# Performance work log

Measured on AMD Instinct MI355X. Metric: run time of the kernel, lower is better.

## Reference

```python
import jax, jax.numpy as jnp
import numpy as np

D_MODEL = 1024
NUM_HEADS = 16
HEAD_DIM = D_MODEL // NUM_HEADS  # 64
B, S = 4, 2048


def setup_inputs() -> dict:
    key = jax.random.key(0)
    ks = jax.random.split(key, 10)
    scale = 1.0 / np.sqrt(D_MODEL)
    x = jax.random.normal(ks[0], (B, S, D_MODEL), dtype=jnp.float32)
    # per-head projection weights stacked over the head axis (matches ModuleList of Linears)
    Wq = jax.random.normal(ks[1], (NUM_HEADS, D_MODEL, HEAD_DIM), dtype=jnp.float32) * scale
    bq = jax.random.normal(ks[2], (NUM_HEADS, HEAD_DIM), dtype=jnp.float32) * 0.01
    Wk = jax.random.normal(ks[3], (NUM_HEADS, D_MODEL, HEAD_DIM), dtype=jnp.float32) * scale
    bk = jax.random.normal(ks[4], (NUM_HEADS, HEAD_DIM), dtype=jnp.float32) * 0.01
    Wv = jax.random.normal(ks[5], (NUM_HEADS, D_MODEL, HEAD_DIM), dtype=jnp.float32) * scale
    bv = jax.random.normal(ks[6], (NUM_HEADS, HEAD_DIM), dtype=jnp.float32) * 0.01
    Wo = jax.random.normal(ks[7], (D_MODEL, D_MODEL), dtype=jnp.float32) * scale
    bo = jax.random.normal(ks[8], (D_MODEL,), dtype=jnp.float32) * 0.01
    return {"hidden_state": x, "Wq": Wq, "bq": bq, "Wk": Wk, "bk": bk,
            "Wv": Wv, "bv": bv, "Wo": Wo, "bo": bo}


def reference(hidden_state, Wq, bq, Wk, bk, Wv, bv, Wo, bo):
    # q,k,v: [B, H, S, E]
    q = jnp.einsum('bsd,hde->bhse', hidden_state, Wq) + bq[None, :, None, :]
    k = jnp.einsum('bsd,hde->bhse', hidden_state, Wk) + bk[None, :, None, :]
    v = jnp.einsum('bsd,hde->bhse', hidden_state, Wv) + bv[None, :, None, :]
    scores = jnp.einsum('bhse,bhte->bhst', q, k) / jnp.sqrt(jnp.asarray(HEAD_DIM, q.dtype))
    weights = jax.nn.softmax(scores, axis=-1)  # [B, H, S, S]
    attn = jnp.einsum('bhst,bhte->bhse', weights, v)  # [B, H, S, E]
    # concat heads along feature dim (head order preserved)
    attn = jnp.transpose(attn, (0, 2, 1, 3)).reshape(hidden_state.shape[0], hidden_state.shape[1], D_MODEL)
    return attn @ Wo + bo
```

## Files before the change

### kernel.cpp

```cpp
#include <hip/hip_runtime.h>

typedef __bf16 bf16x8 __attribute__((ext_vector_type(8)));
typedef float f32x4 __attribute__((ext_vector_type(4)));
typedef unsigned int u32x4 __attribute__((ext_vector_type(4)));
typedef unsigned int u32x2 __attribute__((ext_vector_type(2)));
typedef unsigned short u16x8 __attribute__((ext_vector_type(8)));

#define MFMA_BF16(a, b, c) __builtin_amdgcn_mfma_f32_16x16x32_bf16((a), (b), (c), 0, 0, 0)

#define QSCALE 0.18033688011112043f

__device__ __forceinline__ unsigned short f2bf(float f) {
    unsigned int u = __builtin_bit_cast(unsigned int, f);
    u += 0x7FFFu + ((u >> 16) & 1u);
    return (unsigned short)(u >> 16);
}

__device__ __forceinline__ unsigned int pack_bf16_rne(float a, float b) {
    unsigned int ua = __builtin_bit_cast(unsigned int, a);
    unsigned int ub = __builtin_bit_cast(unsigned int, b);
    ua += 0x7FFFu + ((ua >> 16) & 1u);
    ub += 0x7FFFu + ((ub >> 16) & 1u);
    return __builtin_amdgcn_perm(ub, ua, 0x07060302);
}

#if __has_builtin(__builtin_amdgcn_cvt_pk_bf16_f32)
typedef __bf16 bf16x2 __attribute__((ext_vector_type(2)));
__device__ __forceinline__ unsigned int pack_bf16(float a, float b) {
    return __builtin_bit_cast(unsigned int, __builtin_amdgcn_cvt_pk_bf16_f32(a, b));
}
#else
__device__ __forceinline__ unsigned int pack_bf16(float a, float b) {
    return pack_bf16_rne(a, b);
}
#endif

#if __has_builtin(__builtin_amdgcn_exp2f)
__device__ __forceinline__ float fast_exp2(float x) { return __builtin_amdgcn_exp2f(x); }
#else
__device__ __forceinline__ float fast_exp2(float x) {
    float r;
    asm("v_exp_f32 %0, %1\n\ts_nop 0" : "=v"(r) : "v"(x));
    return r;
}
#endif

__device__ __forceinline__ bf16x8 ldfrag(const unsigned short* p) {
    return __builtin_bit_cast(bf16x8, *(const u32x4*)p);
}

typedef const __attribute__((address_space(1))) void* gas_t;
typedef __attribute__((address_space(3))) void* las_t;
__device__ __forceinline__ void dma16(const unsigned short* g, unsigned short* l) {
    __builtin_amdgcn_global_load_lds((gas_t)(const void*)g, (las_t)(void*)l, 16, 0, 0);
}

__device__ __forceinline__ void pipeline_barrier() {
    __builtin_amdgcn_s_waitcnt(0);
    __syncthreads();
}


__global__ void cvt_x_kernel(const float* __restrict__ in, unsigned short* __restrict__ out) {
    long long t = (long long)blockIdx.x * 256 + threadIdx.x;
    const f32x4* p = (const f32x4*)in + t * 2;
    f32x4 v0 = p[0], v1 = p[1];
    u16x8 o;
    o[0] = f2bf(v0[0]); o[1] = f2bf(v0[1]); o[2] = f2bf(v0[2]); o[3] = f2bf(v0[3]);
    o[4] = f2bf(v1[0]); o[5] = f2bf(v1[1]); o[6] = f2bf(v1[2]); o[7] = f2bf(v1[3]);
    *((u16x8*)out + t) = o;
}

__global__ void cvt_wqkvT_kernel(const float* __restrict__ Wq, const float* __restrict__ Wk,
                                 const float* __restrict__ Wv, unsigned short* __restrict__ WT) {
    int n = blockIdx.x * 256 + threadIdx.x;
    int d0 = blockIdx.y * 8;
    int proj = n >> 10, rem = n & 1023, h = rem >> 6, e = rem & 63;
    const float* W = (proj == 0) ? Wq : (proj == 1) ? Wk : Wv;
    const float* src = W + (size_t)h * 65536 + (size_t)d0 * 64 + e;
    u16x8 o;
#pragma unroll
    for (int j = 0; j < 8; j++) o[j] = f2bf(src[j * 64]);
    *(u16x8*)(WT + (size_t)n * 1024 + d0) = o;
}

__global__ void cvt_woT_kernel(const float* __restrict__ Wo, unsigned short* __restrict__ WoT) {
    int n = blockIdx.x * 256 + threadIdx.x;
    int d0 = blockIdx.y * 8;
    const float* src = Wo + (size_t)d0 * 1024 + n;
    u16x8 o;
#pragma unroll
    for (int j = 0; j < 8; j++) o[j] = f2bf(src[j * 1024]);
    *(u16x8*)(WoT + (size_t)n * 1024 + d0) = o;
}


__global__ __launch_bounds__(256) void gemm_qkv_kernel(
    const unsigned short* __restrict__ A, const unsigned short* __restrict__ BT,
    const float* __restrict__ bq, const float* __restrict__ bk, const float* __restrict__ bv,
    unsigned short* __restrict__ Qo, unsigned short* __restrict__ Ko, unsigned short* __restrict__ VTo) {
    __shared__ unsigned short As[2 * 128 * 32];
    __shared__ unsigned short Bs[2 * 128 * 32];
    const int tid = threadIdx.x;
    const int m0 = blockIdx.y * 128, n0 = blockIdx.x * 128;
    const int w = tid >> 6, lane = tid & 63, lr = lane & 15, quad = lane >> 4;
    const int wy = w >> 1, wx = w & 1;
    f32x4 acc[4][4];
#pragma unroll
    for (int i = 0; i < 4; i++)
#pragma unroll
        for (int j = 0; j < 4; j++) acc[i][j] = (f32x4){0.f, 0.f, 0.f, 0.f};
    const int drow = lane >> 2;
    const int dchunk = (lane & 3) ^ (drow & 3);
    const unsigned short* gA = A + (size_t)(m0 + w * 32 + drow) * 1024 + dchunk * 8;
    const unsigned short* gB = BT + (size_t)(n0 + w * 32 + drow) * 1024 + dchunk * 8;
    const int swav = (w * 32) * 32;
    const int fcol = (quad ^ (lr & 3)) * 8;
    dma16(gA, As + swav);
    dma16(gA + 16 * 1024, As + swav + 16 * 32);
    dma16(gB, Bs + swav);
    dma16(gB + 16 * 1024, Bs + swav + 16 * 32);
#pragma unroll 2
    for (int k0 = 0; k0 < 1024; k0 += 32) {
        const int cur = (k0 >> 5) & 1;
        const unsigned short* cA = As + cur * 4096;
        const unsigned short* cB = Bs + cur * 4096;
        pipeline_barrier();
        bf16x8 af[4], bfr[4];
#pragma unroll
        for (int i = 0; i < 4; i++) af[i] = ldfrag(cA + (wy * 64 + i * 16 + lr) * 32 + fcol);
#pragma unroll
        for (int j = 0; j < 4; j++) bfr[j] = ldfrag(cB + (wx * 64 + j * 16 + lr) * 32 + fcol);
        if (k0 + 32 < 1024) {
            const int nb = (cur ^ 1) * 4096 + swav;
            dma16(gA + k0 + 32, As + nb);
            dma16(gA + k0 + 32 + 16 * 1024, As + nb + 16 * 32);
            dma16(gB + k0 + 32, Bs + nb);
            dma16(gB + k0 + 32 + 16 * 1024, Bs + nb + 16 * 32);
        }
#pragma unroll
        for (int i = 0; i < 4; i++)
#pragma unroll
            for (int j = 0; j < 4; j++) acc[i][j] = MFMA_BF16(af[i], bfr[j], acc[i][j]);
    }
#pragma unroll
    for (int j = 0; j < 4; j++) {
        int n = n0 + wx * 64 + j * 16 + lr;
        int proj = n >> 10, rem = n & 1023, h = rem >> 6, e = rem & 63;
        if (proj == 2) {
            float bb = bv[rem];
#pragma unroll
            for (int i = 0; i < 4; i++) {
                int m = m0 + wy * 64 + i * 16 + quad * 4;
                int batch = m >> 11, s = m & 2047;
                u32x2 pk;
                pk[0] = pack_bf16_rne(acc[i][j][0] + bb, acc[i][j][1] + bb);
                pk[1] = pack_bf16_rne(acc[i][j][2] + bb, acc[i][j][3] + bb);
                *(u32x2*)(VTo + (((size_t)batch * 16 + h) * 64 + e) * 2048 + s) = pk;
            }
        } else {
            const float* bias = (proj == 0) ? bq : bk;
            unsigned short* dst = (proj == 0) ? Qo : Ko;
            float bb = bias[rem];
            float scl = (proj == 0) ? QSCALE : 1.0f;
#pragma unroll
            for (int i = 0; i < 4; i++) {
#pragma unroll
                for (int r = 0; r < 4; r++) {
                    int m = m0 + wy * 64 + i * 16 + quad * 4 + r;
                    int batch = m >> 11, s = m & 2047;
                    dst[(((size_t)batch * 16 + h) * 2048 + s) * 64 + e] = f2bf((acc[i][j][r] + bb) * scl);
                }
            }
        }
    }
}

__global__ __launch_bounds__(256) void gemm_out_kernel(
    const unsigned short* __restrict__ A, const unsigned short* __restrict__ BT,
    const float* __restrict__ bo, float* __restrict__ out) {
    __shared__ unsigned short As[2 * 128 * 32];
    __shared__ unsigned short Bs[2 * 128 * 32];
    const int tid = threadIdx.x;
    const int m0 = blockIdx.y * 128, n0 = blockIdx.x * 128;
    const int w = tid >> 6, lane = tid & 63, lr = lane & 15, quad = lane >> 4;
    const int wy = w >> 1, wx = w & 1;
    f32x4 acc[4][4];
#pragma unroll
    for (int i = 0; i < 4; i++)
#pragma unroll
        for (int j = 0; j < 4; j++) acc[i][j] = (f32x4){0.f, 0.f, 0.f, 0.f};
    const int drow = lane >> 2;
    const int dchunk = (lane & 3) ^ (drow & 3);
    const unsigned short* gA = A + (size_t)(m0 + w * 32 + drow) * 1024 + dchunk * 8;
    const unsigned short* gB = BT + (size_t)(n0 + w * 32 + drow) * 1024 + dchunk * 8;
    const int swav = (w * 32) * 32;
    const int fcol = (quad ^ (lr & 3)) * 8;
    dma16(gA, As + swav);
    dma16(gA + 16 * 1024, As + swav + 16 * 32);
    dma16(gB, Bs + swav);
    dma16(gB + 16 * 1024, Bs + swav + 16 * 32);
#pragma unroll 2
    for (int k0 = 0; k0 < 1024; k0 += 32) {
        const int cur = (k0 >> 5) & 1;
        const unsigned short* cA = As + cur * 4096;
        const unsigned short* cB = Bs + cur * 4096;
        pipeline_barrier();
        bf16x8 af[4], bfr[4];
#pragma unroll
        for (int i = 0; i < 4; i++) af[i] = ldfrag(cA + (wy * 64 + i * 16 + lr) * 32 + fcol);
#pragma unroll
        for (int j = 0; j < 4; j++) bfr[j] = ldfrag(cB + (wx * 64 + j * 16 + lr) * 32 + fcol);
        if (k0 + 32 < 1024) {
            const int nb = (cur ^ 1) * 4096 + swav;
            dma16(gA + k0 + 32, As + nb);
            dma16(gA + k0 + 32 + 16 * 1024, As + nb + 16 * 32);
            dma16(gB + k0 + 32, Bs + nb);
            dma16(gB + k0 + 32 + 16 * 1024, Bs + nb + 16 * 32);
        }
#pragma unroll
        for (int i = 0; i < 4; i++)
#pragma unroll
            for (int j = 0; j < 4; j++) acc[i][j] = MFMA_BF16(af[i], bfr[j], acc[i][j]);
    }
#pragma unroll
    for (int j = 0; j < 4; j++) {
        int n = n0 + wx * 64 + j * 16 + lr;
        float bb = bo[n];
#pragma unroll
        for (int i = 0; i < 4; i++) {
#pragma unroll
            for (int r = 0; r < 4; r++) {
                int m = m0 + wy * 64 + i * 16 + quad * 4 + r;
                out[(size_t)m * 1024 + n] = acc[i][j][r] + bb;
            }
        }
    }
}

#define ST 72
__global__ __launch_bounds__(256, 2) void attn_fa_kernel(
    const unsigned short* __restrict__ Q, const unsigned short* __restrict__ K,
    const unsigned short* __restrict__ VT, unsigned short* __restrict__ Out) {
    __shared__ unsigned short Ps[256 * ST];
    const int bh = blockIdx.x;
    const int q0 = blockIdx.y * 256;
    const int tid = threadIdx.x;
    const int w = tid >> 6, lane = tid & 63, lr = lane & 15, quad = lane >> 4;
    const int W = w * 64;
    const unsigned short* Qh = Q + (size_t)bh * 2048 * 64;
    const unsigned short* Kh = K + (size_t)bh * 2048 * 64;
    const unsigned short* Vh = VT + (size_t)bh * 64 * 2048;

    {
        const unsigned short* g = Qh + (size_t)(q0 + W + lane) * 64;
        unsigned short* s = Ps + (W + lane) * ST;
#pragma unroll
        for (int c = 0; c < 8; c++) *(u32x4*)(s + c * 8) = *(const u32x4*)(g + c * 8);
    }
    bf16x8 qb[4][2];
#pragma unroll
    for (int nt = 0; nt < 4; nt++)
#pragma unroll
        for (int kc = 0; kc < 2; kc++)
            qb[nt][kc] = ldfrag(Ps + (W + nt * 16 + lr) * ST + kc * 32 + quad * 8);

    f32x4 o[4][4];
#pragma unroll
    for (int i = 0; i < 4; i++)
#pragma unroll
        for (int j = 0; j < 4; j++) o[i][j] = (f32x4){0.f, 0.f, 0.f, 0.f};
    float lp[4] = {0.f, 0.f, 0.f, 0.f};

    const unsigned short* gK = Kh + (size_t)lr * 64 + quad * 8;
    const unsigned short* gV = Vh + (size_t)lr * 2048 + quad * 8;

    for (int t0 = 0; t0 < 2048; t0 += 64) {
        bf16x8 ka[2][4];
#pragma unroll
        for (int kc = 0; kc < 2; kc++)
#pragma unroll
            for (int mt = 0; mt < 4; mt++)
                ka[kc][mt] = ldfrag(gK + (size_t)(t0 + mt * 16) * 64 + kc * 32);

        f32x4 sc[4][4];
#pragma unroll
        for (int mt = 0; mt < 4; mt++)
#pragma unroll
            for (int nt = 0; nt < 4; nt++) sc[mt][nt] = (f32x4){0.f, 0.f, 0.f, 0.f};
#pragma unroll
        for (int kc = 0; kc < 2; kc++)
#pragma unroll
            for (int mt = 0; mt < 4; mt++)
#pragma unroll
                for (int nt = 0; nt < 4; nt++)
                    sc[mt][nt] = MFMA_BF16(ka[kc][mt], qb[nt][kc], sc[mt][nt]);

        bf16x8 vb[2][4];
#pragma unroll
        for (int kc = 0; kc < 2; kc++)
#pragma unroll
            for (int et = 0; et < 4; et++)
                vb[kc][et] = ldfrag(gV + (size_t)(et * 16) * 2048 + t0 + kc * 32);

#pragma unroll
        for (int nt = 0; nt < 4; nt++) {
            unsigned short* prow = Ps + (W + nt * 16 + lr) * ST + quad * 4;
#pragma unroll
            for (int mt = 0; mt < 4; mt++) {
                float p0 = fast_exp2(sc[mt][nt][0]);
                float p1 = fast_exp2(sc[mt][nt][1]);
                float p2 = fast_exp2(sc[mt][nt][2]);
                float p3 = fast_exp2(sc[mt][nt][3]);
                lp[nt] += (p0 + p1) + (p2 + p3);
                u32x2 pk;
                pk[0] = pack_bf16(p0, p1);
                pk[1] = pack_bf16(p2, p3);
                *(u32x2*)(prow + mt * 16) = pk;
            }
        }

#pragma unroll
        for (int kc = 0; kc < 2; kc++) {
            bf16x8 pa[4];
#pragma unroll
            for (int nt = 0; nt < 4; nt++)
                pa[nt] = ldfrag(Ps + (W + nt * 16 + lr) * ST + kc * 32 + quad * 8);
#pragma unroll
            for (int nt = 0; nt < 4; nt++)
#pragma unroll
                for (int et = 0; et < 4; et++)
                    o[nt][et] = MFMA_BF16(pa[nt], vb[kc][et], o[nt][et]);
        }
    }

#pragma unroll
    for (int nt = 0; nt < 4; nt++) {
        float l = lp[nt];
        l += __shfl_xor(l, 16, 64);
        l += __shfl_xor(l, 32, 64);
        lp[nt] = l;
    }

    const int h = bh & 15, b = bh >> 4;
#pragma unroll
    for (int nt = 0; nt < 4; nt++) {
#pragma unroll
        for (int r = 0; r < 4; r++) {
            float l = __shfl(lp[nt], quad * 4 + r, 16);
            float inv = 1.0f / l;
            int s = q0 + W + nt * 16 + quad * 4 + r;
#pragma unroll
            for (int et = 0; et < 4; et++) {
                int col = h * 64 + et * 16 + lr;
                Out[((size_t)(b * 2048 + s)) * 1024 + col] = f2bf(o[nt][et][r] * inv);
            }
        }
    }
}


extern "C" void kernel_launch(void* const* d_in, const int* in_sizes, int n_in,
                              void* d_out, int out_size, void* d_ws, size_t ws_size,
                              hipStream_t stream) {
    const float* x  = (const float*)d_in[0];
    const float* Wq = (const float*)d_in[1];
    const float* bq = (const float*)d_in[2];
    const float* Wk = (const float*)d_in[3];
    const float* bk = (const float*)d_in[4];
    const float* Wv = (const float*)d_in[5];
    const float* bv = (const float*)d_in[6];
    const float* Wo = (const float*)d_in[7];
    const float* bo = (const float*)d_in[8];
    float* out = (float*)d_out;

    char* ws = (char*)d_ws;
    unsigned short* xb    = (unsigned short*)(ws);
    unsigned short* WqkvT = (unsigned short*)(ws + 16777216);
    unsigned short* WoT   = (unsigned short*)(ws + 23068672);
    unsigned short* Qb    = (unsigned short*)(ws + 25165824);
    unsigned short* Kb    = (unsigned short*)(ws + 41943040);
    unsigned short* VTb   = (unsigned short*)(ws + 58720256);
    unsigned short* attn  = xb;

    cvt_x_kernel<<<dim3(4096), dim3(256), 0, stream>>>(x, xb);
    cvt_wqkvT_kernel<<<dim3(12, 128), dim3(256), 0, stream>>>(Wq, Wk, Wv, WqkvT);
    cvt_woT_kernel<<<dim3(4, 128), dim3(256), 0, stream>>>(Wo, WoT);
    gemm_qkv_kernel<<<dim3(24, 64), dim3(256), 0, stream>>>(xb, WqkvT, bq, bk, bv, Qb, Kb, VTb);
    attn_fa_kernel<<<dim3(64, 8), dim3(256), 0, stream>>>(Qb, Kb, VTb, attn);
    gemm_out_kernel<<<dim3(8, 64), dim3(256), 0, stream>>>(attn, WoT, bo, out);
}
```

Measured before the change: 345.9 us.

## Double-buffer K/V tiles in LDS via async DMA in attention kernel

Each attention workgroup now stages K and V^T tiles into a double-buffered, XOR-swizzled shared-memory buffer using async global-to-LDS copies, prefetching the next tile while computing the current one. Before this, every wave loaded K/V fragments straight from global memory, and the four waves fetched the same tiles redundantly. The change adds 32KB of LDS per block and a barrier per iteration, which could reduce occupancy or add sync stalls.

```diff
diff --git a/kernel.cpp b/kernel.cpp
--- a/kernel.cpp
+++ b/kernel.cpp
@@ -242,6 +242,8 @@
 __global__ __launch_bounds__(256, 2) void attn_fa_kernel(
     const unsigned short* __restrict__ Q, const unsigned short* __restrict__ K,
     const unsigned short* __restrict__ VT, unsigned short* __restrict__ Out) {
+    __shared__ unsigned short Ks[2 * 64 * 64];
+    __shared__ unsigned short Vs[2 * 64 * 64];
     __shared__ unsigned short Ps[256 * ST];
     const int bh = blockIdx.x;
     const int q0 = blockIdx.y * 256;
@@ -252,6 +254,16 @@
     const unsigned short* Kh = K + (size_t)bh * 2048 * 64;
     const unsigned short* Vh = VT + (size_t)bh * 64 * 2048;
 
+    const int drow = lane >> 3;
+    const int dchunk = (lane & 7) ^ drow;
+    const unsigned short* gK = Kh + (size_t)(w * 16 + drow) * 64 + dchunk * 8;
+    const unsigned short* gV = Vh + (size_t)(w * 16 + drow) * 2048 + dchunk * 8;
+    const int swav = (w * 16) * 64;
+    dma16(gK, Ks + swav);
+    dma16(gK + 8 * 64, Ks + swav + 8 * 64);
+    dma16(gV, Vs + swav);
+    dma16(gV + 8 * 2048, Vs + swav + 8 * 64);
+
     {
         const unsigned short* g = Qh + (size_t)(q0 + W + lane) * 64;
         unsigned short* s = Ps + (W + lane) * ST;
@@ -272,16 +284,27 @@
         for (int j = 0; j < 4; j++) o[i][j] = (f32x4){0.f, 0.f, 0.f, 0.f};
     float lp[4] = {0.f, 0.f, 0.f, 0.f};
 
-    const unsigned short* gK = Kh + (size_t)lr * 64 + quad * 8;
-    const unsigned short* gV = Vh + (size_t)lr * 2048 + quad * 8;
-
     for (int t0 = 0; t0 < 2048; t0 += 64) {
-        bf16x8 ka[2][4];
+        const int cur = (t0 >> 6) & 1;
+        const unsigned short* cK = Ks + cur * 4096;
+        const unsigned short* cV = Vs + cur * 4096;
+        pipeline_barrier();
+        bf16x8 ka[2][4], vb[2][4];
 #pragma unroll
         for (int kc = 0; kc < 2; kc++)
 #pragma unroll
-            for (int mt = 0; mt < 4; mt++)
-                ka[kc][mt] = ldfrag(gK + (size_t)(t0 + mt * 16) * 64 + kc * 32);
+            for (int mt = 0; mt < 4; mt++) {
+                int fc = ((kc * 4 + quad) ^ (lr & 7)) * 8;
+                ka[kc][mt] = ldfrag(cK + (mt * 16 + lr) * 64 + fc);
+                vb[kc][mt] = ldfrag(cV + (mt * 16 + lr) * 64 + fc);
+            }
+        if (t0 + 64 < 2048) {
+            const int nb = (cur ^ 1) * 4096 + swav;
+            dma16(gK + (size_t)(t0 + 64) * 64, Ks + nb);
+            dma16(gK + (size_t)(t0 + 64) * 64 + 8 * 64, Ks + nb + 8 * 64);
+            dma16(gV + t0 + 64, Vs + nb);
+            dma16(gV + t0 + 64 + 8 * 2048, Vs + nb + 8 * 64);
+        }
 
         f32x4 sc[4][4];
 #pragma unroll
@@ -295,13 +318,6 @@
 #pragma unroll
                 for (int nt = 0; nt < 4; nt++)
                     sc[mt][nt] = MFMA_BF16(ka[kc][mt], qb[nt][kc], sc[mt][nt]);
-
-        bf16x8 vb[2][4];
-#pragma unroll
-        for (int kc = 0; kc < 2; kc++)
-#pragma unroll
-            for (int et = 0; et < 4; et++)
-                vb[kc][et] = ldfrag(gV + (size_t)(et * 16) * 2048 + t0 + kc * 32);
 
 #pragma unroll
         for (int nt = 0; nt < 4; nt++) {
```

After: 307.4 us. 11.1% less time.

## Stage K/V tiles in shared memory with swizzle, use 128-thread attention blocks

Applied to the files above, without the earlier changes.

The attention kernel now loads each 64-key K and V tile into LDS with async DMA and reads MFMA fragments from there, where before each wave fetched them straight from global memory. Blocks shrink to 128 threads (two waves, 128 queries) and the grid doubles. The Q/P scratch drops its padded stride for an XOR swizzle to avoid bank conflicts. The GEMM loops lose their unroll-2 pragma. The goal is to share K/V loads across waves and cut redundant global traffic, at the cost of a barrier per tile and no double buffering.

```diff
diff --git a/kernel.cpp b/kernel.cpp
--- a/kernel.cpp
+++ b/kernel.cpp
@@ -120,7 +120,6 @@
     dma16(gA + 16 * 1024, As + swav + 16 * 32);
     dma16(gB, Bs + swav);
     dma16(gB + 16 * 1024, Bs + swav + 16 * 32);
-#pragma unroll 2
     for (int k0 = 0; k0 < 1024; k0 += 32) {
         const int cur = (k0 >> 5) & 1;
         const unsigned short* cA = As + cur * 4096;
@@ -200,7 +199,6 @@
     dma16(gA + 16 * 1024, As + swav + 16 * 32);
     dma16(gB, Bs + swav);
     dma16(gB + 16 * 1024, Bs + swav + 16 * 32);
-#pragma unroll 2
     for (int k0 = 0; k0 < 1024; k0 += 32) {
         const int cur = (k0 >> 5) & 1;
         const unsigned short* cA = As + cur * 4096;
@@ -238,13 +236,14 @@
     }
 }
 
-#define ST 72
-__global__ __launch_bounds__(256, 2) void attn_fa_kernel(
+__global__ __launch_bounds__(128, 2) void attn_fa_kernel(
     const unsigned short* __restrict__ Q, const unsigned short* __restrict__ K,
     const unsigned short* __restrict__ VT, unsigned short* __restrict__ Out) {
-    __shared__ unsigned short Ps[256 * ST];
+    __shared__ unsigned short Ks[64 * 64];
+    __shared__ unsigned short Vs[64 * 64];
+    __shared__ unsigned short Ps[128 * 64];
     const int bh = blockIdx.x;
-    const int q0 = blockIdx.y * 256;
+    const int q0 = blockIdx.y * 128;
     const int tid = threadIdx.x;
     const int w = tid >> 6, lane = tid & 63, lr = lane & 15, quad = lane >> 4;
     const int W = w * 64;
@@ -252,18 +251,27 @@
     const unsigned short* Kh = K + (size_t)bh * 2048 * 64;
     const unsigned short* Vh = VT + (size_t)bh * 64 * 2048;
 
+    const int drow = lane >> 3;
+    const int dchunk = (lane & 7) ^ drow;
+    const unsigned short* gK = Kh + (size_t)(w * 32 + drow) * 64 + dchunk * 8;
+    const unsigned short* gV = Vh + (size_t)(w * 32 + drow) * 2048 + dchunk * 8;
+    unsigned short* sK = Ks + (w * 32) * 64;
+    unsigned short* sV = Vs + (w * 32) * 64;
+
     {
-        const unsigned short* g = Qh + (size_t)(q0 + W + lane) * 64;
-        unsigned short* s = Ps + (W + lane) * ST;
-#pragma unroll
-        for (int c = 0; c < 8; c++) *(u32x4*)(s + c * 8) = *(const u32x4*)(g + c * 8);
-    }
+        const unsigned short* g = Qh + (size_t)(q0 + tid) * 64;
+        unsigned short* s = Ps + tid * 64;
+        const int rx = tid & 7;
+#pragma unroll
+        for (int c = 0; c < 8; c++) *(u32x4*)(s + ((c ^ rx) * 8)) = *(const u32x4*)(g + c * 8);
+    }
+    __syncthreads();
     bf16x8 qb[4][2];
 #pragma unroll
     for (int nt = 0; nt < 4; nt++)
 #pragma unroll
         for (int kc = 0; kc < 2; kc++)
-            qb[nt][kc] = ldfrag(Ps + (W + nt * 16 + lr) * ST + kc * 32 + quad * 8);
+            qb[nt][kc] = ldfrag(Ps + (W + nt * 16 + lr) * 64 + (((kc * 4 + quad) ^ (lr & 7)) * 8));
 
     f32x4 o[4][4];
 #pragma unroll
@@ -272,16 +280,24 @@
         for (int j = 0; j < 4; j++) o[i][j] = (f32x4){0.f, 0.f, 0.f, 0.f};
     float lp[4] = {0.f, 0.f, 0.f, 0.f};
 
-    const unsigned short* gK = Kh + (size_t)lr * 64 + quad * 8;
-    const unsigned short* gV = Vh + (size_t)lr * 2048 + quad * 8;
-
     for (int t0 = 0; t0 < 2048; t0 += 64) {
-        bf16x8 ka[2][4];
+        __syncthreads();
+#pragma unroll
+        for (int i = 0; i < 4; i++) {
+            dma16(gK + (size_t)(t0 + i * 8) * 64, sK + i * 8 * 64);
+            dma16(gV + (t0 + (size_t)i * 8 * 2048) - (size_t)0, sV + i * 8 * 64);
+        }
+        pipeline_barrier();
+
+        bf16x8 ka[2][4], vb[2][4];
 #pragma unroll
         for (int kc = 0; kc < 2; kc++)
 #pragma unroll
-            for (int mt = 0; mt < 4; mt++)
-                ka[kc][mt] = ldfrag(gK + (size_t)(t0 + mt * 16) * 64 + kc * 32);
+            for (int mt = 0; mt < 4; mt++) {
+                int fc = ((kc * 4 + quad) ^ (lr & 7)) * 8;
+                ka[kc][mt] = ldfrag(Ks + (mt * 16 + lr) * 64 + fc);
+                vb[kc][mt] = ldfrag(Vs + (mt * 16 + lr) * 64 + fc);
+            }
 
         f32x4 sc[4][4];
 #pragma unroll
@@ -296,16 +312,10 @@
                 for (int nt = 0; nt < 4; nt++)
                     sc[mt][nt] = MFMA_BF16(ka[kc][mt], qb[nt][kc], sc[mt][nt]);
 
-        bf16x8 vb[2][4];
-#pragma unroll
-        for (int kc = 0; kc < 2; kc++)
-#pragma unroll
-            for (int et = 0; et < 4; et++)
-                vb[kc][et] = ldfrag(gV + (size_t)(et * 16) * 2048 + t0 + kc * 32);
-
 #pragma unroll
         for (int nt = 0; nt < 4; nt++) {
-            unsigned short* prow = Ps + (W + nt * 16 + lr) * ST + quad * 4;
+            unsigned short* prow = Ps + (W + nt * 16 + lr) * 64 + (quad & 1) * 4;
+            const int rx = lr & 7;
 #pragma unroll
             for (int mt = 0; mt < 4; mt++) {
                 float p0 = fast_exp2(sc[mt][nt][0]);
@@ -316,7 +326,7 @@
                 u32x2 pk;
                 pk[0] = pack_bf16(p0, p1);
                 pk[1] = pack_bf16(p2, p3);
-                *(u32x2*)(prow + mt * 16) = pk;
+                *(u32x2*)(prow + (((2 * mt + (quad >> 1)) ^ rx) * 8)) = pk;
             }
         }
 
@@ -325,7 +335,7 @@
             bf16x8 pa[4];
 #pragma unroll
             for (int nt = 0; nt < 4; nt++)
-                pa[nt] = ldfrag(Ps + (W + nt * 16 + lr) * ST + kc * 32 + quad * 8);
+                pa[nt] = ldfrag(Ps + (W + nt * 16 + lr) * 64 + (((kc * 4 + quad) ^ (lr & 7)) * 8));
 #pragma unroll
             for (int nt = 0; nt < 4; nt++)
 #pragma unroll
@@ -387,6 +397,6 @@
     cvt_wqkvT_kernel<<<dim3(12, 128), dim3(256), 0, stream>>>(Wq, Wk, Wv, WqkvT);
     cvt_woT_kernel<<<dim3(4, 128), dim3(256), 0, stream>>>(Wo, WoT);
     gemm_qkv_kernel<<<dim3(24, 64), dim3(256), 0, stream>>>(xb, WqkvT, bq, bk, bv, Qb, Kb, VTb);
-    attn_fa_kernel<<<dim3(64, 8), dim3(256), 0, stream>>>(Qb, Kb, VTb, attn);
+    attn_fa_kernel<<<dim3(64, 16), dim3(128), 0, stream>>>(Qb, Kb, VTb, attn);
     gemm_out_kernel<<<dim3(8, 64), dim3(256), 0, stream>>>(attn, WoT, bo, out);
 }
```

Result: faster. 300.0 us (-13.3%).
